# Optimization experiments

Hardware: AMD Instinct MI355X
Metric: run time of the kernel (lower is better)

## Reference

```python
import jax, jax.numpy as jnp
import numpy as np

W_SEG = 2048   # segment_length w
R = 4          # dilation r
H = 16         # num_attention_heads


def setup_inputs() -> dict:
    key = jax.random.key(0)
    k0, k1, k2 = jax.random.split(key, 3)
    B, S, Hid = 2, 8192, 1024
    X = jax.random.normal(k0, (B, S, Hid), dtype=jnp.float32)
    Wq = jax.random.normal(k1, (Hid, Hid), dtype=jnp.float32) * 0.02
    bq = jnp.zeros((Hid,), jnp.float32)
    Wkv = jax.random.normal(k2, (Hid, 2 * Hid), dtype=jnp.float32) * 0.02
    bkv = jnp.zeros((2 * Hid,), jnp.float32)
    return {"X": X, "Wq": Wq, "bq": bq, "Wkv": Wkv, "bkv": bkv}


def reference(X, Wq, bq, Wkv, bkv):
    B, S, Hid = X.shape
    D = Hid // H                      # head dim
    num_points = W_SEG // R           # tokens kept per segment
    num_seg = S // W_SEG
    scale = 1.0 / np.sqrt(D).astype(np.float32)

    q = (X @ Wq + bq).reshape(B, S, H, D)
    kv = (X @ Wkv + bkv).reshape(B, S, 2, H, D)
    k, v = kv[:, :, 0], kv[:, :, 1]

    # dilated base indices: segment offset + r-strided points -> [num_seg*num_points]
    base = (jnp.arange(num_seg)[:, None] * W_SEG
            + jnp.arange(num_points)[None, :] * R).reshape(-1)
    shift = jnp.arange(H) % R                       # per-head shift
    idx = base[None, :] + shift[:, None]            # [H, T']
    Tq = idx.shape[1]
    idxT = idx.T                                    # [T', H]
    head_ix = jnp.arange(H)[None, :]                # [1, H] -> broadcasts with idxT

    # per-head dilated gather: sparse[b, t, h, d] = full[b, idx[h, t], h, d]
    sq = q[:, idxT, head_ix, :]                     # [B, T', H, D]
    sk = k[:, idxT, head_ix, :]
    sv = v[:, idxT, head_ix, :]

    sq = sq.reshape(B, num_seg, num_points, H, D)
    sk = sk.reshape(B, num_seg, num_points, H, D)
    sv = sv.reshape(B, num_seg, num_points, H, D)

    # per-segment (non-causal) attention, same math as flash_attn_kvpacked_func
    scores = jnp.einsum('bsqhd,bskhd->bshqk', sq, sk) * scale
    probs = jax.nn.softmax(scores, axis=-1)
    ctx = jnp.einsum('bshqk,bskhd->bsqhd', probs, sv)
    ctx = ctx.reshape(B, Tq, H, D)

    # scatter back into zeros at the gathered positions (unique per head)
    out = jnp.zeros((B, S, H, D), ctx.dtype).at[:, idxT, head_ix, :].set(ctx)
    return out.reshape(B, S, Hid)
```

## Files before the change

### kernel.cpp

```cpp
#include <hip/hip_runtime.h>

typedef unsigned short u16;
typedef unsigned int   u32;
typedef __bf16 bf16x8 __attribute__((ext_vector_type(8)));
typedef float  f32x4  __attribute__((ext_vector_type(4)));
typedef short  s16x4  __attribute__((ext_vector_type(4)));

#define QSCALE 0.125f

__device__ __forceinline__ u16 f2bf(float f) {
  union { float f; u32 u; } a; a.f = f;
  u32 u = a.u;
  u = (u + 0x7FFFu + ((u >> 16) & 1u)) >> 16;
  return (u16)u;
}

__device__ __forceinline__ void async16(const void* g, void* l) {
  __builtin_amdgcn_global_load_lds(
      (const __attribute__((address_space(1))) void*)g,
      (__attribute__((address_space(3))) void*)l, 16, 0, 0);
}

__global__ __launch_bounds__(256) void pack_x(const float* __restrict__ X,
                                              u16* __restrict__ Xp) {
  __shared__ uint4 lds[2048];
  int bx  = blockIdx.x;
  int ks4 = bx & 7;
  int Mt  = (bx >> 3) & 31;
  int r   = bx >> 8;
  int bseg = Mt >> 2;
  int p0   = (Mt & 3) * 128;
  int tid = threadIdx.x;
  int lane16 = tid & 15;
  int r16    = tid >> 4;
  int ksl = lane16 >> 2, kc = lane16 & 3;
  int xsw = (ksl * 4 + kc) & 7;
#pragma unroll
  for (int it = 0; it < 8; ++it) {
    int m_local = it * 16 + r16;
    const float* src = X + (size_t)(bseg * 2048 + (p0 + m_local) * 4 + r) * 1024
                         + ks4 * 128 + lane16 * 8;
    float4 v0 = *(const float4*)src;
    float4 v1 = *(const float4*)(src + 4);
    uint4 o;
    o.x = f2bf(v0.x) | ((u32)f2bf(v0.y) << 16);
    o.y = f2bf(v0.z) | ((u32)f2bf(v0.w) << 16);
    o.z = f2bf(v1.x) | ((u32)f2bf(v1.y) << 16);
    o.w = f2bf(v1.z) | ((u32)f2bf(v1.w) << 16);
    lds[ksl * 512 + it * 64 + kc * 16 + (r16 ^ xsw)] = o;
  }
  __syncthreads();
  u16* outb = Xp + (size_t)r * 4194304 + (size_t)Mt * 131072 + (size_t)ks4 * 16384;
#pragma unroll
  for (int jt = 0; jt < 8; ++jt) {
    int g = jt * 256 + tid;
    int ksl2 = g >> 9, v = g & 511;
    int kc2 = (v >> 4) & 3, mm2 = v & 15;
    uint4 o = lds[ksl2 * 512 + (v & ~15) + (mm2 ^ ((ksl2 * 4 + kc2) & 7))];
    *(uint4*)(outb + (size_t)g * 8) = o;
  }
}

__global__ __launch_bounds__(256) void pack_w(const float* __restrict__ Wq,
                                              const float* __restrict__ Wkv,
                                              u16* __restrict__ Wp) {
  __shared__ float tile[32][65];
  int bx = blockIdx.x;
  int ks = bx & 31; int rem = bx >> 5;
  int hh = rem & 3; rem >>= 2;
  int t  = rem % 3; int r = rem / 3;
  int h  = hh * 4 + r;
  const float* src; int rs, cb;
  if (t == 0)      { src = Wq;  rs = 1024; cb = h * 64; }
  else if (t == 1) { src = Wkv; rs = 2048; cb = h * 64; }
  else             { src = Wkv; rs = 2048; cb = 1024 + h * 64; }
  int tid = threadIdx.x;
  {
    int kk = tid >> 3, dd = (tid & 7) << 3;
    const float* s0 = src + (size_t)(ks * 32 + kk) * rs + cb + dd;
    float4 a = *(const float4*)s0;
    float4 c = *(const float4*)(s0 + 4);
    tile[kk][dd + 0] = a.x; tile[kk][dd + 1] = a.y;
    tile[kk][dd + 2] = a.z; tile[kk][dd + 3] = a.w;
    tile[kk][dd + 4] = c.x; tile[kk][dd + 5] = c.y;
    tile[kk][dd + 6] = c.z; tile[kk][dd + 7] = c.w;
  }
  __syncthreads();
  {
    int d = tid >> 2, kc = tid & 3;
    float sc = (t == 0) ? QSCALE : 1.0f;
    u32 w[4];
#pragma unroll
    for (int j = 0; j < 4; ++j) {
      u16 lo = f2bf(tile[kc * 8 + 2 * j][d] * sc);
      u16 hi = f2bf(tile[kc * 8 + 2 * j + 1][d] * sc);
      w[j] = (u32)lo | ((u32)hi << 16);
    }
    int n = t * 256 + hh * 64 + d;
    int Nt = n >> 7, nt = (n >> 4) & 7, nn = n & 15;
    size_t off = (size_t)r * 786432 + (size_t)Nt * 131072 +
                 (size_t)ks * 4096 + nt * 512 + kc * 128 + nn * 8;
    uint4 o; o.x = w[0]; o.y = w[1]; o.z = w[2]; o.w = w[3];
    *(uint4*)(Wp + off) = o;
  }
}

__global__ __launch_bounds__(256) void pack_bias(const float* __restrict__ bq,
                                                 const float* __restrict__ bkv,
                                                 float* __restrict__ bp) {
  int idx = blockIdx.x * 256 + threadIdx.x;
  int r = idx / 768, n = idx % 768;
  int t = n >> 8, hh = (n >> 6) & 3, d = n & 63;
  int h = hh * 4 + r;
  float v = (t == 0) ? bq[h * 64 + d] * QSCALE
          : (t == 1) ? bkv[h * 64 + d]
                     : bkv[1024 + h * 64 + d];
  bp[idx] = v;
}

__global__ __launch_bounds__(256, 3) void gemm1(const u16* __restrict__ Xp,
                                                const u16* __restrict__ Wp,
                                                const float* __restrict__ bp,
                                                u16* __restrict__ Qd,
                                                u16* __restrict__ Kd,
                                                u16* __restrict__ Vd) {
  __shared__ u16 ldsA[4096];
  __shared__ u16 ldsB[4096];
  int bx = blockIdx.x;
  int r = bx / 192; int rem = bx % 192;
  int Mtile = rem / 6, Ntile = rem % 6;
  int tid = threadIdx.x, w = tid >> 6, lane = tid & 63;
  int wr = w >> 1, wc = w & 1;
  int l15 = lane & 15, l4 = lane >> 4;

  const u16* Asrc = Xp + (size_t)r * 4194304 + (size_t)Mtile * 131072 +
                    w * 1024 + lane * 8;
  const u16* Bsrc = Wp + (size_t)r * 786432 + (size_t)Ntile * 131072 +
                    w * 1024 + lane * 8;

  f32x4 acc[4][4] = {};
  for (int ks = 0; ks < 32; ++ks) {
    const u16* a = Asrc + ks * 4096;
    const u16* b = Bsrc + ks * 4096;
    async16(a,       &ldsA[w * 1024]);
    async16(a + 512, &ldsA[w * 1024 + 512]);
    async16(b,       &ldsB[w * 1024]);
    async16(b + 512, &ldsB[w * 1024 + 512]);
    __syncthreads();
    bf16x8 af[4], bf[4];
#pragma unroll
    for (int i = 0; i < 4; ++i)
      af[i] = *(const bf16x8*)&ldsA[((wr * 4 + i) * 64 + lane) * 8];
#pragma unroll
    for (int j = 0; j < 4; ++j)
      bf[j] = *(const bf16x8*)&ldsB[((wc * 4 + j) * 64 + lane) * 8];
#pragma unroll
    for (int i = 0; i < 4; ++i)
#pragma unroll
      for (int j = 0; j < 4; ++j)
        acc[i][j] = __builtin_amdgcn_mfma_f32_16x16x32_bf16(af[i], bf[j],
                                                            acc[i][j], 0, 0, 0);
    __syncthreads();
  }

#pragma unroll
  for (int j = 0; j < 4; ++j) {
    int n = Ntile * 128 + wc * 64 + j * 16 + l15;
    float bias = bp[r * 768 + n];
    int t = n >> 8, hh = (n >> 6) & 3, d = n & 63;
    int h = hh * 4 + r;
    u16* T = (t == 0) ? Qd : ((t == 1) ? Kd : Vd);
#pragma unroll
    for (int i = 0; i < 4; ++i) {
      int mrow = Mtile * 128 + wr * 64 + i * 16 + l4 * 4;
#pragma unroll
      for (int reg = 0; reg < 4; ++reg) {
        int m = mrow + reg;
        int bseg = m >> 9, p = m & 511;
        size_t idx = ((size_t)(bseg * 16 + h) * 512 + p) * 64 + d;
        T[idx] = f2bf(acc[i][j][reg] + bias);
      }
    }
  }
}

__global__ __launch_bounds__(512, 4) void attn(const u16* __restrict__ Qd,
                                               const u16* __restrict__ Kd,
                                               const u16* __restrict__ Vd,
                                               float* __restrict__ out) {
  __shared__ u16 ldsK[128 * 72];
  __shared__ u16 ldsV[64 * 136];
  int bx = blockIdx.x;
  int unit = bx >> 2, qq = bx & 3;
  int b = unit >> 6, seg = (unit >> 4) & 3, h = unit & 15;
  int tid = threadIdx.x, w = tid >> 6, lane = tid & 63;
  int l15 = lane & 15, l4 = lane >> 4;
  const u16* Qu = Qd + (size_t)unit * 32768;
  const u16* Ku = Kd + (size_t)unit * 32768;
  const u16* Vu = Vd + (size_t)unit * 32768;

  int q0 = qq * 128 + w * 16;
  bf16x8 qf[2];
#pragma unroll
  for (int hf = 0; hf < 2; ++hf)
    qf[hf] = *(const bf16x8*)(Qu + (q0 + l15) * 64 + hf * 32 + l4 * 8);

  f32x4 O[4] = {};
  float lrun = 0.f;

  int c0 = tid, c1 = 512 + tid;
  int kp0 = c0 >> 3, kd0 = c0 & 7;
  int kp1 = c1 >> 3, kd1 = c1 & 7;
  int vd0 = (c0 & 7) << 3, vd1 = (c1 & 7) << 3;

  uint4 kreg0 = *(const uint4*)(Ku + c0 * 8);
  uint4 kreg1 = *(const uint4*)(Ku + c1 * 8);
  uint4 vreg0 = *(const uint4*)(Vu + c0 * 8);
  uint4 vreg1 = *(const uint4*)(Vu + c1 * 8);

  for (int ch = 0; ch < 4; ++ch) {
    __syncthreads();
    *(uint4*)&ldsK[kp0 * 72 + kd0 * 8] = kreg0;
    *(uint4*)&ldsK[kp1 * 72 + kd1 * 8] = kreg1;
    {
      u32 ww0[4] = {vreg0.x, vreg0.y, vreg0.z, vreg0.w};
      u32 ww1[4] = {vreg1.x, vreg1.y, vreg1.z, vreg1.w};
#pragma unroll
      for (int j = 0; j < 4; ++j) {
        ldsV[(vd0 + 2 * j) * 136 + kp0]     = (u16)(ww0[j] & 0xFFFFu);
        ldsV[(vd0 + 2 * j + 1) * 136 + kp0] = (u16)(ww0[j] >> 16);
        ldsV[(vd1 + 2 * j) * 136 + kp1]     = (u16)(ww1[j] & 0xFFFFu);
        ldsV[(vd1 + 2 * j + 1) * 136 + kp1] = (u16)(ww1[j] >> 16);
      }
    }
    __syncthreads();
    if (ch < 3) {
      const u16* Ksn = Ku + (ch + 1) * 8192;
      const u16* Vsn = Vu + (ch + 1) * 8192;
      kreg0 = *(const uint4*)(Ksn + c0 * 8);
      kreg1 = *(const uint4*)(Ksn + c1 * 8);
      vreg0 = *(const uint4*)(Vsn + c0 * 8);
      vreg1 = *(const uint4*)(Vsn + c1 * 8);
    }

    float csum = 0.f;
    s16x4 pk[8];
#pragma unroll
    for (int kt = 0; kt < 8; ++kt) {
      bf16x8 a0 = *(const bf16x8*)&ldsK[(kt * 16 + l15) * 72 + l4 * 8];
      bf16x8 a1 = *(const bf16x8*)&ldsK[(kt * 16 + l15) * 72 + 32 + l4 * 8];
      f32x4 s = __builtin_amdgcn_mfma_f32_16x16x32_bf16(
          a0, qf[0], (f32x4){0.f, 0.f, 0.f, 0.f}, 0, 0, 0);
      s = __builtin_amdgcn_mfma_f32_16x16x32_bf16(a1, qf[1], s, 0, 0, 0);
      float e0 = __expf(s[0]);
      float e1 = __expf(s[1]);
      float e2 = __expf(s[2]);
      float e3 = __expf(s[3]);
      csum += (e0 + e1) + (e2 + e3);
      s16x4 pv;
      pv[0] = (short)(__float_as_uint(e0) >> 16);
      pv[1] = (short)(__float_as_uint(e1) >> 16);
      pv[2] = (short)(__float_as_uint(e2) >> 16);
      pv[3] = (short)(__float_as_uint(e3) >> 16);
      pk[kt] = pv;
    }
    csum += __shfl_xor(csum, 16, 64);
    csum += __shfl_xor(csum, 32, 64);
    lrun += csum;
#pragma unroll
    for (int kt = 0; kt < 8; ++kt)
#pragma unroll
      for (int dn = 0; dn < 4; ++dn) {
        s16x4 vb = *(const s16x4*)&ldsV[(dn * 16 + l15) * 136 + kt * 16 + l4 * 4];
        O[dn] = __builtin_amdgcn_mfma_f32_16x16x16bf16_1k(pk[kt], vb,
                                                          O[dn], 0, 0, 0);
      }
  }

  {
    float rl = __builtin_amdgcn_rcpf(lrun);
#pragma unroll
    for (int reg = 0; reg < 4; ++reg) {
      float rr = __shfl(rl, l4 * 4 + reg, 64);
      int p = q0 + l4 * 4 + reg;
      int spos = seg * 2048 + p * 4 + (h & 3);
      size_t base = ((size_t)(b * 8192 + spos)) * 1024 + h * 64 + l15;
#pragma unroll
      for (int dn = 0; dn < 4; ++dn)
        out[base + dn * 16] = O[dn][reg] * rr;
    }
  }

  {
    int row_i = bx * 32 + (tid >> 4);
    int sub = tid & 15;
    int rr = row_i & 3;
    float4 z = {0.f, 0.f, 0.f, 0.f};
    float* rowp = out + (size_t)row_i * 1024 + sub * 4;
#pragma unroll
    for (int hz = 0; hz < 16; ++hz) {
      if ((hz & 3) == rr) continue;
      *(float4*)(rowp + hz * 64) = z;
    }
  }
}

extern "C" void kernel_launch(void* const* d_in, const int* in_sizes, int n_in,
                              void* d_out, int out_size, void* d_ws, size_t ws_size,
                              hipStream_t stream) {
  (void)in_sizes; (void)n_in; (void)ws_size; (void)out_size;
  const float* X   = (const float*)d_in[0];
  const float* Wq  = (const float*)d_in[1];
  const float* bq  = (const float*)d_in[2];
  const float* Wkv = (const float*)d_in[3];
  const float* bkv = (const float*)d_in[4];
  float* out = (float*)d_out;
  char* ws = (char*)d_ws;
  u16*  Xp = (u16*)(ws);
  u16*  Wp = (u16*)(ws + 33554432);
  float* bp = (float*)(ws + 39845888);
  u16*  Qd = (u16*)(ws + 39858176);
  u16*  Kd = (u16*)(ws + 48246784);
  u16*  Vd = (u16*)(ws + 56635392);

  pack_x   <<<1024, 256, 0, stream>>>(X, Xp);
  pack_w   <<<1536, 256, 0, stream>>>(Wq, Wkv, Wp);
  pack_bias<<<12,   256, 0, stream>>>(bq, bkv, bp);
  gemm1    <<<768,  256, 0, stream>>>(Xp, Wp, bp, Qd, Kd, Vd);
  attn     <<<512,  512, 0, stream>>>(Qd, Kd, Vd, out);
}
```

Baseline: 206.5 us.

## Stage gemm1 epilogue through LDS for vectorized stores and remap blocks per XCD

The GEMM epilogue previously wrote scattered 2-byte bf16 values straight to global memory. It now stages each 16-row slab in LDS and writes back with 16-byte vector stores along contiguous head-dim rows. The block index is also remapped so that blocks landing on the same XCD share the same dilation group r and half of the M tiles, which should improve L2 reuse of X and W. The cost is extra LDS traffic and barriers in the epilogue.

```diff
diff --git a/kernel.cpp b/kernel.cpp
--- a/kernel.cpp
+++ b/kernel.cpp
@@ -124,11 +124,15 @@
                                                 u16* __restrict__ Qd,
                                                 u16* __restrict__ Kd,
                                                 u16* __restrict__ Vd) {
-  __shared__ u16 ldsA[4096];
-  __shared__ u16 ldsB[4096];
+  __shared__ u16 ldsAB[8192];
+  u16* ldsA = ldsAB;
+  u16* ldsB = ldsAB + 4096;
   int bx = blockIdx.x;
-  int r = bx / 192; int rem = bx % 192;
-  int Mtile = rem / 6, Ntile = rem % 6;
+  int xcd = bx & 7;
+  int idx = bx >> 3;
+  int r = xcd >> 1;
+  int Mtile = (xcd & 1) * 16 + (idx / 6);
+  int Ntile = idx % 6;
   int tid = threadIdx.x, w = tid >> 6, lane = tid & 63;
   int wr = w >> 1, wc = w & 1;
   int l15 = lane & 15, l4 = lane >> 4;
@@ -163,24 +167,32 @@
     __syncthreads();
   }
 
-#pragma unroll
-  for (int j = 0; j < 4; ++j) {
-    int n = Ntile * 128 + wc * 64 + j * 16 + l15;
-    float bias = bp[r * 768 + n];
-    int t = n >> 8, hh = (n >> 6) & 3, d = n & 63;
-    int h = hh * 4 + r;
-    u16* T = (t == 0) ? Qd : ((t == 1) ? Kd : Vd);
-#pragma unroll
-    for (int i = 0; i < 4; ++i) {
-      int mrow = Mtile * 128 + wr * 64 + i * 16 + l4 * 4;
-#pragma unroll
-      for (int reg = 0; reg < 4; ++reg) {
-        int m = mrow + reg;
-        int bseg = m >> 9, p = m & 511;
-        size_t idx = ((size_t)(bseg * 16 + h) * 512 + p) * 64 + d;
-        T[idx] = f2bf(acc[i][j][reg] + bias);
-      }
-    }
+  int nb = Ntile * 128 + wc * 64;
+  int t = nb >> 8, hh = (nb >> 6) & 3;
+  int h = hh * 4 + r;
+  u16* T = (t == 0) ? Qd : ((t == 1) ? Kd : Vd);
+  float biasv[4];
+#pragma unroll
+  for (int j = 0; j < 4; ++j) biasv[j] = bp[r * 768 + nb + j * 16 + l15];
+
+  u16* eb = ldsAB + w * 1152;
+  int rrow = lane >> 2, seg = lane & 3;
+#pragma unroll
+  for (int i = 0; i < 4; ++i) {
+    __syncthreads();
+#pragma unroll
+    for (int j = 0; j < 4; ++j)
+#pragma unroll
+      for (int reg = 0; reg < 4; ++reg)
+        eb[(l4 * 4 + reg) * 72 + j * 16 + l15] = f2bf(acc[i][j][reg] + biasv[j]);
+    __syncthreads();
+    uint4 d0 = *(const uint4*)&eb[rrow * 72 + seg * 16];
+    uint4 d1 = *(const uint4*)&eb[rrow * 72 + seg * 16 + 8];
+    int m = Mtile * 128 + wr * 64 + i * 16 + rrow;
+    int bseg = m >> 9, p = m & 511;
+    size_t off = ((size_t)(bseg * 16 + h) * 512 + p) * 64 + seg * 16;
+    *(uint4*)(T + off) = d0;
+    *(uint4*)(T + off + 8) = d1;
   }
 }
 
```

Measured after the change: 199.3 us. -3.5%, faster.
